# Performance work log

Measured on AMD Instinct MI355X. Metric: run time of the kernel, lower is better.

The kernel has to match this reference:

```python
import jax, jax.numpy as jnp
import numpy as np

BN_EPS = 1e-5
SQ_EPS = 1e-12


def _mlp(x, Wa, ba, g, b, Wb, bb):
    # Linear -> BatchNorm1d (eval mode, running mean=0 var=1) -> ReLU -> Linear
    h = x @ Wa + ba
    h = h * (g / jnp.sqrt(1.0 + BN_EPS)) + b
    h = jax.nn.relu(h)
    return h @ Wb + bb


def _signed_sqrt(x):
    # sqrt(relu(x)) - sqrt(relu(-x)); tiny eps keeps grads finite at exact zeros
    return jnp.sqrt(jax.nn.relu(x) + SQ_EPS) - jnp.sqrt(jax.nn.relu(-x) + SQ_EPS)


def setup_inputs() -> dict:
    G, NPG, H, POLY, L, T, TASKS, DEG = 1024, 16, 128, 16, 3, 1048576, 1, 8
    N = G * NPG
    P = G * NPG * NPG
    E = N * DEG
    key = jax.random.key(0)
    ks = iter(jax.random.split(key, 64))

    def nrm(shape, s):
        return jax.random.normal(next(ks), shape, jnp.float32) * s

    w = 0.06  # ~xavier scale for 128-dim layers
    inp = {
        'pair_x': nrm((P, POLY), 1.0),
        'diag_x': nrm((N, POLY), 1.0),
        'node_h': nrm((N, H), 1.0),
        'edge_h': nrm((E, H), 1.0),
        'W_pair': nrm((POLY, H), 0.12),
        'W_diag': nrm((POLY, H), 0.12),
        'Wd': nrm((2 * H, TASKS), w),
        'bd': jnp.zeros((TASKS,), jnp.float32),
    }
    for p, ind in (('m1', H), ('m2', H), ('up', 2 * H)):
        inp[p + '_Wa'] = nrm((L, ind, H), w)
        inp[p + '_ba'] = jnp.zeros((L, H), jnp.float32)
        inp[p + '_g'] = jnp.ones((L, H), jnp.float32)
        inp[p + '_b'] = jnp.zeros((L, H), jnp.float32)
        inp[p + '_Wb'] = nrm((L, H, H), w)
        inp[p + '_bb'] = jnp.zeros((L, H), jnp.float32)
    inp['edge_pos'] = jax.random.randint(next(ks), (E,), 0, P)
    n = jnp.arange(N)
    inp['diag_pos'] = (n // NPG) * NPG * NPG + (n % NPG) * NPG + (n % NPG)
    # graph-local triples: base pair block of the graph + random local pair ids
    tg = jax.random.randint(next(ks), (T,), 0, G) * (NPG * NPG)
    loc = jax.random.randint(next(ks), (3, T), 0, NPG * NPG)
    inp['triple_index'] = tg[None, :] + loc
    inp['batch'] = jnp.repeat(jnp.arange(G), NPG)
    inp['pair_x_batch'] = jnp.repeat(jnp.arange(G), NPG * NPG)
    inp['ptr'] = jnp.arange(G + 1) * NPG
    inp['pair_x_ptr'] = jnp.arange(G + 1) * (NPG * NPG)
    return inp


def reference(pair_x, diag_x, node_h, edge_h, W_pair, W_diag,
              m1_Wa, m1_ba, m1_g, m1_b, m1_Wb, m1_bb,
              m2_Wa, m2_ba, m2_g, m2_b, m2_Wb, m2_bb,
              up_Wa, up_ba, up_g, up_b, up_Wb, up_bb,
              Wd, bd,
              edge_pos, diag_pos, triple_index, batch, pair_x_batch, ptr, pair_x_ptr):
    P = pair_x.shape[0]
    # InitLayer: coalesce-add of pair, edge and diagonal (node) contributions
    pair_h = pair_x @ W_pair                             # [P, H]
    pair_h = pair_h.at[edge_pos].add(edge_h)
    pair_h = pair_h.at[diag_pos].add(node_h + diag_x @ W_diag)
    idx0, idx1, idx2 = triple_index[0], triple_index[1], triple_index[2]
    L = m1_Wa.shape[0]
    for l in range(L):  # fixed small layer count
        h1 = _mlp(pair_h, m1_Wa[l], m1_ba[l], m1_g[l], m1_b[l], m1_Wb[l], m1_bb[l])
        h2 = _mlp(pair_h, m2_Wa[l], m2_ba[l], m2_g[l], m2_b[l], m2_Wb[l], m2_bb[l])
        x3 = h1[idx1] * h2[idx2]                         # [T, H] gather-multiply
        agg = jax.ops.segment_sum(x3, idx0, num_segments=P)  # scatter_add
        agg = _signed_sqrt(agg)                          # use_sqrt=True
        h = jnp.concatenate([pair_h, agg], axis=-1)      # [P, 2H]
        pair_h = _mlp(h, up_Wa[l], up_ba[l], up_g[l], up_b[l], up_Wb[l], up_bb[l]) + pair_h
    G = ptr.shape[0] - 1
    agg_all = jax.ops.segment_sum(pair_h, pair_x_batch, num_segments=G)
    agg_diag = jax.ops.segment_sum(pair_h[diag_pos], batch, num_segments=G)
    agg_off = agg_all - agg_diag
    node_sz = jnp.diff(ptr)[:, None].astype(pair_h.dtype)
    pair_sz = jnp.diff(pair_x_ptr)[:, None].astype(pair_h.dtype)
    agg_off = agg_off / jnp.maximum(pair_sz - node_sz, 1.0)  # 'mean' pooling
    agg_diag = agg_diag / node_sz
    graph_h = jnp.concatenate([agg_diag, agg_off], axis=-1)  # [G, 2H]
    return graph_h @ Wd + bd                             # output decoder
```

## Files before the change

kernel.cpp:

```cpp
#include <hip/hip_runtime.h>
#include <hip/hip_bf16.h>

#define H 128
#define POLY 16
#define PPG 256
#define GNUM 1024
#define PTOT 262144
#define NTOT 16384
#define ETOT 131072
#define TTOT 1048576

#define NCHUNK 4
#define GPC (GNUM / NCHUNK)
#define ROWS (PTOT / NCHUNK)

#define NB PTOT

#define XS 136

typedef __attribute__((ext_vector_type(8))) _Float16       f16x8;
typedef __attribute__((ext_vector_type(8))) unsigned short ushort8;
typedef __attribute__((ext_vector_type(4))) float          f32x4;

__device__ __forceinline__ unsigned short f2h(float f) {
    _Float16 h = (_Float16)f;
    return __builtin_bit_cast(unsigned short, h);
}
__device__ __forceinline__ float h2f(unsigned short u) {
    _Float16 h = __builtin_bit_cast(_Float16, u);
    return (float)h;
}
__device__ __forceinline__ void split2(float x, unsigned short& h, unsigned short& l)
{
    h = f2h(x);
    l = f2h(x - h2f(h));
}
__device__ __forceinline__ f16x8 ldf16(const unsigned short* p)
{
    return __builtin_bit_cast(f16x8, *(const ushort8*)p);
}

__global__ __launch_bounds__(256)
void k_init_pair(const float* __restrict__ px, const float* __restrict__ Wp,
                 float* __restrict__ ph)
{
    const int tid = threadIdx.x;
    const int c4 = (tid & 31) * 4;
    float4 w[POLY];
#pragma unroll
    for (int k = 0; k < POLY; ++k) w[k] = *(const float4*)(Wp + k * H + c4);
    const size_t r0 = (size_t)blockIdx.x * 64 + (tid >> 5) * 8;
#pragma unroll
    for (int rr = 0; rr < 8; ++rr) {
        const size_t p = r0 + rr;
        const float4* xp = (const float4*)(px + p * POLY);
        const float4 v0 = xp[0], v1 = xp[1], v2 = xp[2], v3 = xp[3];
        const float x[POLY] = {v0.x, v0.y, v0.z, v0.w, v1.x, v1.y, v1.z, v1.w,
                               v2.x, v2.y, v2.z, v2.w, v3.x, v3.y, v3.z, v3.w};
        float4 a = make_float4(0.f, 0.f, 0.f, 0.f);
#pragma unroll
        for (int k = 0; k < POLY; ++k) {
            a.x = fmaf(x[k], w[k].x, a.x);
            a.y = fmaf(x[k], w[k].y, a.y);
            a.z = fmaf(x[k], w[k].z, a.z);
            a.w = fmaf(x[k], w[k].w, a.w);
        }
        *(float4*)(ph + p * H + c4) = a;
    }
}

__global__ __launch_bounds__(256)
void k_edge(const float* __restrict__ eh, const int* __restrict__ epos, float* ph)
{
    const int tid = threadIdx.x;
    const size_t e = (size_t)blockIdx.x * 2 + (tid >> 7);
    const int c = tid & 127;
    atomicAdd(&ph[(size_t)epos[e] * H + c], eh[e * H + c]);
}

__global__ __launch_bounds__(256)
void k_diag(const float* __restrict__ nh, const float* __restrict__ dx,
            const float* __restrict__ Wdg, const int* __restrict__ dpos, float* ph)
{
    const int tid = threadIdx.x;
    const int c4 = (tid & 31) * 4;
    float4 w[POLY];
#pragma unroll
    for (int k = 0; k < POLY; ++k) w[k] = *(const float4*)(Wdg + k * H + c4);
    const size_t n0 = (size_t)blockIdx.x * 64 + (tid >> 5) * 8;
#pragma unroll
    for (int rr = 0; rr < 8; ++rr) {
        const size_t n = n0 + rr;
        const float4* xp = (const float4*)(dx + n * POLY);
        const float4 v0 = xp[0], v1 = xp[1], v2 = xp[2], v3 = xp[3];
        const float x[POLY] = {v0.x, v0.y, v0.z, v0.w, v1.x, v1.y, v1.z, v1.w,
                               v2.x, v2.y, v2.z, v2.w, v3.x, v3.y, v3.z, v3.w};
        const float4 nv = *(const float4*)(nh + n * H + c4);
        float4 a = nv;
#pragma unroll
        for (int k = 0; k < POLY; ++k) {
            a.x = fmaf(x[k], w[k].x, a.x);
            a.y = fmaf(x[k], w[k].y, a.y);
            a.z = fmaf(x[k], w[k].z, a.z);
            a.w = fmaf(x[k], w[k].w, a.w);
        }
        float* dst = ph + (size_t)dpos[n] * H + c4;
        const float4 old = *(const float4*)dst;
        a.x += old.x; a.y += old.y; a.z += old.z; a.w += old.w;
        *(float4*)dst = a;
    }
}

__global__ __launch_bounds__(1024)
void k_zero(int* counts) { counts[blockIdx.x * 1024 + threadIdx.x] = 0; }

__global__ __launch_bounds__(256)
void k_count(const int* __restrict__ i0, int* counts)
{
    const int t = blockIdx.x * 256 + threadIdx.x;
    atomicAdd(&counts[i0[t]], 1);
}

__global__ __launch_bounds__(1024)
void k_scan1(const int* __restrict__ counts, int* __restrict__ offs, int* __restrict__ bsum)
{
    __shared__ int s[1024];
    const int t = threadIdx.x;
    const int i = blockIdx.x * 1024 + t;
    const int v = counts[i];
    s[t] = v;
    __syncthreads();
    for (int d = 1; d < 1024; d <<= 1) {
        int add = (t >= d) ? s[t - d] : 0;
        __syncthreads();
        s[t] += add;
        __syncthreads();
    }
    offs[i] = s[t] - v;
    if (t == 1023) bsum[blockIdx.x] = s[1023];
}

__global__ __launch_bounds__(256)
void k_scan2(const int* __restrict__ bsum, int* __restrict__ bbase)
{
    __shared__ int s[256];
    const int t = threadIdx.x;
    const int v = bsum[t];
    s[t] = v;
    __syncthreads();
    for (int d = 1; d < 256; d <<= 1) {
        int add = (t >= d) ? s[t - d] : 0;
        __syncthreads();
        s[t] += add;
        __syncthreads();
    }
    bbase[t] = s[t] - v;
}

__global__ __launch_bounds__(1024)
void k_scan3(int* __restrict__ offs, const int* __restrict__ bbase, int* __restrict__ cursor)
{
    const int i = blockIdx.x * 1024 + threadIdx.x;
    const int o = offs[i] + bbase[blockIdx.x];
    offs[i] = o;
    cursor[i] = o;
    if (i == 0) offs[NB] = TTOT;
}

__global__ __launch_bounds__(256)
void k_fill(const int* __restrict__ i0, const int* __restrict__ i1,
            const int* __restrict__ i2, int* cursor, unsigned short* __restrict__ tri16)
{
    const int t = blockIdx.x * 256 + threadIdx.x;
    const int a0 = i0[t];
    const int pos = atomicAdd(&cursor[a0], 1);
    tri16[pos] = (unsigned short)((i1[t] & 255) | ((i2[t] & 255) << 8));
}

__device__ __forceinline__ void stage2(const float* __restrict__ src,
                                       unsigned short* Xh, unsigned short* Xl, int tid)
{
#pragma unroll
    for (int it = 0; it < 4; ++it) {
        const int r = (tid >> 4) + it * 16;
        const int c = (tid & 15) * 8;
        const float4 v0 = *(const float4*)(src + (size_t)r * H + c);
        const float4 v1 = *(const float4*)(src + (size_t)r * H + c + 4);
        const float x[8] = {v0.x, v0.y, v0.z, v0.w, v1.x, v1.y, v1.z, v1.w};
        ushort8 vh, vl;
#pragma unroll
        for (int j = 0; j < 8; ++j) {
            unsigned short hh, ll;
            split2(x[j], hh, ll);
            vh[j] = hh; vl[j] = ll;
        }
        *(ushort8*)(Xh + r * XS + c) = vh;
        *(ushort8*)(Xl + r * XS + c) = vl;
    }
}

#define MFMA16F(A, B, C) __builtin_amdgcn_mfma_f32_16x16x32_f16(A, B, C, 0, 0, 0)

__device__ __forceinline__ void gemm2(const unsigned short* Xh, const unsigned short* Xl,
                                      const unsigned short* __restrict__ wp,
                                      const int rt, const int cb, const int lane,
                                      f32x4 (&acc)[2][4])
{
    const int arow = lane & 15, akb = (lane >> 4) * 8;
#pragma unroll
    for (int kc = 0; kc < 4; ++kc) {
        const int kin = kc * 32 + akb;
        f16x8 ah[2], al[2];
#pragma unroll
        for (int s = 0; s < 2; ++s) {
            const int ro = (rt + s * 16 + arow) * XS + kin;
            ah[s] = ldf16(Xh + ro);
            al[s] = ldf16(Xl + ro);
        }
#pragma unroll
        for (int j = 0; j < 4; ++j) {
            const unsigned short* bp = wp + (size_t)(kc * 8 + cb + j) * 1024 + lane * 8;
            const f16x8 bh = ldf16(bp);
            const f16x8 bl = ldf16(bp + 512);
#pragma unroll
            for (int s = 0; s < 2; ++s) {
                acc[s][j] = MFMA16F(ah[s], bh, acc[s][j]);
                acc[s][j] = MFMA16F(al[s], bh, acc[s][j]);
                acc[s][j] = MFMA16F(ah[s], bl, acc[s][j]);
                acc[s][j] = MFMA16F(al[s], bl, acc[s][j]);
            }
        }
    }
}

__global__ __launch_bounds__(256)
void k_mlp_m12(const float* __restrict__ x1,
               const unsigned short* __restrict__ wa1, const float* __restrict__ ba1,
               const float* __restrict__ gg1, const float* __restrict__ bsh1,
               const unsigned short* __restrict__ wb1, const float* __restrict__ bb1,
               float* __restrict__ out1,
               const unsigned short* __restrict__ wa2, const float* __restrict__ ba2,
               const float* __restrict__ gg2, const float* __restrict__ bsh2,
               const unsigned short* __restrict__ wb2, const float* __restrict__ bb2,
               float* __restrict__ out2)
{
    __shared__ unsigned short Xh[64 * XS], Xl[64 * XS];

    const int tid = threadIdx.x, lane = tid & 63, wid = tid >> 6;
    const int sel = blockIdx.x & 1;
    const size_t row0 = (size_t)(blockIdx.x >> 1) * 64;

    const unsigned short* wa = sel ? wa2 : wa1;
    const unsigned short* wb = sel ? wb2 : wb1;
    const float* ba  = sel ? ba2  : ba1;
    const float* gg  = sel ? gg2  : gg1;
    const float* bsh = sel ? bsh2 : bsh1;
    const float* bb  = sel ? bb2  : bb1;
    float* out = sel ? out2 : out1;

    const int rt = (wid >> 1) * 32;
    const int cb = (wid & 1) * 4;

    f32x4 acc[2][4];
#pragma unroll
    for (int s = 0; s < 2; ++s)
#pragma unroll
        for (int j = 0; j < 4; ++j)
#pragma unroll
            for (int q = 0; q < 4; ++q) acc[s][j][q] = 0.f;

    stage2(x1 + row0 * H, Xh, Xl, tid);
    __syncthreads();
    gemm2(Xh, Xl, wa, rt, cb, lane, acc);
    __syncthreads();

    const float inv_s = rsqrtf(1.0f + 1e-5f);
    const int crow = (lane >> 4) * 4, ccol = lane & 15;
#pragma unroll
    for (int j = 0; j < 4; ++j) {
        const int col = (cb + j) * 16 + ccol;
        const float g  = gg[col] * inv_s;
        const float a_ = ba[col];
        const float b_ = bsh[col];
#pragma unroll
        for (int s = 0; s < 2; ++s)
#pragma unroll
            for (int q = 0; q < 4; ++q) {
                float t = fmaf(acc[s][j][q] + a_, g, b_);
                t = fmaxf(t, 0.f);
                unsigned short hh, ll;
                split2(t, hh, ll);
                const int ro = (rt + s * 16 + crow + q) * XS + col;
                Xh[ro] = hh; Xl[ro] = ll;
                acc[s][j][q] = 0.f;
            }
    }
    __syncthreads();

    gemm2(Xh, Xl, wb, rt, cb, lane, acc);

#pragma unroll
    for (int j = 0; j < 4; ++j) {
        const int col = (cb + j) * 16 + ccol;
        const float bbv = bb[col];
#pragma unroll
        for (int s = 0; s < 2; ++s)
#pragma unroll
            for (int q = 0; q < 4; ++q) {
                const int row = rt + s * 16 + crow + q;
                out[(row0 + row) * H + col] = acc[s][j][q] + bbv;
            }
    }
}

__global__ __launch_bounds__(256)
void k_mlp_up(const float* __restrict__ x1, const float* __restrict__ x2,
              const unsigned short* __restrict__ wpa,
              const float* __restrict__ ba, const float* __restrict__ gg,
              const float* __restrict__ bsh,
              const unsigned short* __restrict__ wpb, const float* __restrict__ bb,
              float* __restrict__ out)
{
    __shared__ unsigned short Xh[64 * XS], Xl[64 * XS];

    const int tid = threadIdx.x, lane = tid & 63, wid = tid >> 6;
    const size_t row0 = (size_t)blockIdx.x * 64;
    const int rt = (wid >> 1) * 32;
    const int cb = (wid & 1) * 4;

    f32x4 acc[2][4];
#pragma unroll
    for (int s = 0; s < 2; ++s)
#pragma unroll
        for (int j = 0; j < 4; ++j)
#pragma unroll
            for (int q = 0; q < 4; ++q) acc[s][j][q] = 0.f;

    stage2(x1 + row0 * H, Xh, Xl, tid);
    __syncthreads();
    gemm2(Xh, Xl, wpa, rt, cb, lane, acc);
    __syncthreads();
    stage2(x2 + row0 * H, Xh, Xl, tid);
    __syncthreads();
    gemm2(Xh, Xl, wpa + 32 * 1024, rt, cb, lane, acc);
    __syncthreads();

    const float inv_s = rsqrtf(1.0f + 1e-5f);
    const int crow = (lane >> 4) * 4, ccol = lane & 15;
#pragma unroll
    for (int j = 0; j < 4; ++j) {
        const int col = (cb + j) * 16 + ccol;
        const float g  = gg[col] * inv_s;
        const float a_ = ba[col];
        const float b_ = bsh[col];
#pragma unroll
        for (int s = 0; s < 2; ++s)
#pragma unroll
            for (int q = 0; q < 4; ++q) {
                float t = fmaf(acc[s][j][q] + a_, g, b_);
                t = fmaxf(t, 0.f);
                unsigned short hh, ll;
                split2(t, hh, ll);
                const int ro = (rt + s * 16 + crow + q) * XS + col;
                Xh[ro] = hh; Xl[ro] = ll;
                acc[s][j][q] = 0.f;
            }
    }
    __syncthreads();

    gemm2(Xh, Xl, wpb, rt, cb, lane, acc);

#pragma unroll
    for (int j = 0; j < 4; ++j) {
        const int col = (cb + j) * 16 + ccol;
        const float bbv = bb[col];
#pragma unroll
        for (int s = 0; s < 2; ++s)
#pragma unroll
            for (int q = 0; q < 4; ++q) {
                const int row = rt + s * 16 + crow + q;
                float o = acc[s][j][q] + bbv + x1[(row0 + row) * H + col];
                out[(row0 + row) * H + col] = o;
            }
    }
}

__global__ __launch_bounds__(64)
void k_prepack2(const float* __restrict__ W, int lstride,
                unsigned short* __restrict__ outp, int ostride)
{
    const int l = blockIdx.y;
    const float* w = W + (size_t)l * lstride;
    unsigned short* o = outp + (size_t)l * ostride + (size_t)blockIdx.x * 1024;
    const int lane = threadIdx.x;
    const int kbase = (blockIdx.x >> 3) * 32 + (lane >> 4) * 8;
    const int col   = (blockIdx.x & 7) * 16 + (lane & 15);
    ushort8 vh, vl;
#pragma unroll
    for (int j = 0; j < 8; ++j) {
        unsigned short hh, ll;
        split2(w[(size_t)(kbase + j) * H + col], hh, ll);
        vh[j] = hh; vl[j] = ll;
    }
    *(ushort8*)(o + lane * 8)       = vh;
    *(ushort8*)(o + 512 + lane * 8) = vl;
}

__global__ __launch_bounds__(256)
void k_triple_s(const float* __restrict__ h1, const float* __restrict__ h2,
                const unsigned short* __restrict__ tri16,
                const int* __restrict__ offs,
                float* __restrict__ aggout)
{
    const int lane = threadIdx.x & 63;
    const int lp   = blockIdx.x * 4 + (threadIdx.x >> 6);
    const int start = offs[lp], end = offs[lp + 1];
    const size_t base = (size_t)(lp >> 8) * PPG * H + lane * 2;
    float ax = 0.f, ay = 0.f;
    unsigned us = (start < end) ? tri16[start] : 0u;
    for (int t = start; t < end; ++t) {
        const unsigned usn = (t + 1 < end) ? tri16[t + 1] : 0u;
        const float2 a = *(const float2*)&h1[base + (size_t)(us & 255u) * H];
        const float2 b = *(const float2*)&h2[base + (size_t)(us >> 8) * H];
        ax = fmaf(a.x, b.x, ax);
        ay = fmaf(a.y, b.y, ay);
        us = usn;
    }
    float2 r;
    r.x = sqrtf(fmaxf(ax, 0.f) + 1e-12f) - sqrtf(fmaxf(-ax, 0.f) + 1e-12f);
    r.y = sqrtf(fmaxf(ay, 0.f) + 1e-12f) - sqrtf(fmaxf(-ay, 0.f) + 1e-12f);
    *(float2*)&aggout[(size_t)lp * H + lane * 2] = r;
}

__global__ __launch_bounds__(256)
void k_pool(const float* __restrict__ ph, const float* __restrict__ Wd,
            const float* __restrict__ bd, float* __restrict__ out)
{
    const int g = blockIdx.x;
    const int tid = threadIdx.x;
    const int c = tid & 127, half = tid >> 7;
    const size_t base = (size_t)g * PPG * H;
    float s = 0.f;
    for (int r = half * 128; r < half * 128 + 128; ++r)
        s += ph[base + (size_t)r * H + c];
    __shared__ float sother[128];
    __shared__ float red[128];
    if (half) sother[c] = s;
    __syncthreads();
    if (!half) {
        const float tot = s + sother[c];
        float d = 0.f;
#pragma unroll
        for (int i = 0; i < 16; ++i)
            d += ph[base + (size_t)(i * 17) * H + c];
        const float diag = d * (1.f / 16.f);
        const float offv = (tot - d) * (1.f / 240.f);
        red[c] = fmaf(diag, Wd[c], offv * Wd[128 + c]);
    }
    __syncthreads();
    if (tid < 64) {
        float r = red[tid] + red[tid + 64];
#pragma unroll
        for (int off = 32; off; off >>= 1) r += __shfl_down(r, off);
        if (tid == 0) out[g] = r + bd[0];
    }
}

extern "C" void kernel_launch(void* const* d_in, const int* in_sizes, int n_in,
                              void* d_out, int out_size, void* d_ws, size_t ws_size,
                              hipStream_t stream)
{
    (void)in_sizes; (void)n_in; (void)out_size;
    const size_t OFF_PH  = 0;
    const size_t OFF_HA  = 134217728;
    const size_t OFF_HB  = 167772160;
    const size_t OFF_AGG = 201326592;
    const size_t OFF_TRI = 234881024;
    const size_t OFF_INT = 236978176;
    const size_t OFF_WP  = 240128000;
    const size_t NEED    = OFF_WP + 1376256;
    if (ws_size < NEED) return;

    const float* pair_x = (const float*)d_in[0];
    const float* diag_x = (const float*)d_in[1];
    const float* node_h = (const float*)d_in[2];
    const float* edge_h = (const float*)d_in[3];
    const float* W_pair = (const float*)d_in[4];
    const float* W_diag = (const float*)d_in[5];
    const float* Wd     = (const float*)d_in[6];
    const float* bd     = (const float*)d_in[7];
    const float* mW[3][6];
    for (int p = 0; p < 3; ++p)
        for (int q = 0; q < 6; ++q)
            mW[p][q] = (const float*)d_in[8 + p * 6 + q];
    const int* edge_pos = (const int*)d_in[26];
    const int* diag_pos = (const int*)d_in[27];
    const int* tri_idx  = (const int*)d_in[28];

    char* w = (char*)d_ws;
    float*          ph   = (float*)(w + OFF_PH);
    float*          hA   = (float*)(w + OFF_HA);
    float*          hB   = (float*)(w + OFF_HB);
    float*          aggC = (float*)(w + OFF_AGG);
    unsigned short* tri16 = (unsigned short*)(w + OFF_TRI);
    int*            counts = (int*)(w + OFF_INT);
    int*            offs   = counts + NB;
    int*            cursor = offs + NB + 8;
    int*            bsum   = cursor + NB;
    int*            bbase  = bsum + 256;
    unsigned short* wp   = (unsigned short*)(w + OFF_WP);

    const int WPL = 229376;

    k_init_pair<<<PTOT / 64, 256, 0, stream>>>(pair_x, W_pair, ph);
    k_edge<<<ETOT / 2, 256, 0, stream>>>(edge_h, edge_pos, ph);
    k_diag<<<NTOT / 64, 256, 0, stream>>>(node_h, diag_x, W_diag, diag_pos, ph);

    k_prepack2<<<dim3(32, 3), 64, 0, stream>>>(mW[0][0], 16384, wp + 0,      WPL);
    k_prepack2<<<dim3(32, 3), 64, 0, stream>>>(mW[0][4], 16384, wp + 32768,  WPL);
    k_prepack2<<<dim3(32, 3), 64, 0, stream>>>(mW[1][0], 16384, wp + 65536,  WPL);
    k_prepack2<<<dim3(32, 3), 64, 0, stream>>>(mW[1][4], 16384, wp + 98304,  WPL);
    k_prepack2<<<dim3(64, 3), 64, 0, stream>>>(mW[2][0], 32768, wp + 131072, WPL);
    k_prepack2<<<dim3(32, 3), 64, 0, stream>>>(mW[2][4], 16384, wp + 196608, WPL);

    k_zero<<<NB / 1024, 1024, 0, stream>>>(counts);
    k_count<<<TTOT / 256, 256, 0, stream>>>(tri_idx, counts);
    k_scan1<<<NB / 1024, 1024, 0, stream>>>(counts, offs, bsum);
    k_scan2<<<1, 256, 0, stream>>>(bsum, bbase);
    k_scan3<<<NB / 1024, 1024, 0, stream>>>(offs, bbase, cursor);
    k_fill<<<TTOT / 256, 256, 0, stream>>>(tri_idx, tri_idx + TTOT, tri_idx + 2 * TTOT,
                                           cursor, tri16);

    for (int l = 0; l < 3; ++l) {
        const unsigned short* wl = wp + (size_t)l * WPL;
        for (int c = 0; c < NCHUNK; ++c) {
            const float* phc = ph + (size_t)c * ROWS * H;
            k_mlp_m12<<<ROWS / 64 * 2, 256, 0, stream>>>(phc,
                wl + 0,      mW[0][1] + l * 128, mW[0][2] + l * 128, mW[0][3] + l * 128,
                wl + 32768,  mW[0][5] + l * 128, hA,
                wl + 65536,  mW[1][1] + l * 128, mW[1][2] + l * 128, mW[1][3] + l * 128,
                wl + 98304,  mW[1][5] + l * 128, hB);
            k_triple_s<<<ROWS / 4, 256, 0, stream>>>(hA, hB, tri16,
                                                     offs + (size_t)c * ROWS, aggC);
            k_mlp_up<<<ROWS / 64, 256, 0, stream>>>(phc, aggC,
                wl + 131072, mW[2][1] + l * 128, mW[2][2] + l * 128, mW[2][3] + l * 128,
                wl + 196608, mW[2][5] + l * 128, (float*)phc);
        }
    }
    k_pool<<<GNUM, 256, 0, stream>>>(ph, Wd, bd, (float*)d_out);
}
```

Measured before the change: 1.757 ms.

## Fuse next chunk's m1/m2 MLP with current chunk's update MLP launch

The two MLP kernels become device helper functions, and a new combined kernel is added. Its first third of blocks runs the update MLP for the current chunk and the remaining blocks run the m1/m2 MLPs for the next chunk, or for chunk 0 of the next layer. The first m1/m2 call is moved before the loop. This is meant to cut launch gaps and give the GPU more independent blocks per launch, so the update-MLP tail overlaps with the next chunk's work. The cost is more register and scheduling pressure in one larger kernel, plus more complex chunk and layer index bookkeeping.

New measurement: 1.695 ms. 3.6% less time.

```diff
diff --git a/kernel.cpp b/kernel.cpp
--- a/kernel.cpp
+++ b/kernel.cpp
@@ -233,22 +233,20 @@
     }
 }
 
-__global__ __launch_bounds__(256)
-void k_mlp_m12(const float* __restrict__ x1,
-               const unsigned short* __restrict__ wa1, const float* __restrict__ ba1,
-               const float* __restrict__ gg1, const float* __restrict__ bsh1,
-               const unsigned short* __restrict__ wb1, const float* __restrict__ bb1,
-               float* __restrict__ out1,
-               const unsigned short* __restrict__ wa2, const float* __restrict__ ba2,
-               const float* __restrict__ gg2, const float* __restrict__ bsh2,
-               const unsigned short* __restrict__ wb2, const float* __restrict__ bb2,
-               float* __restrict__ out2)
-{
-    __shared__ unsigned short Xh[64 * XS], Xl[64 * XS];
-
-    const int tid = threadIdx.x, lane = tid & 63, wid = tid >> 6;
-    const int sel = blockIdx.x & 1;
-    const size_t row0 = (size_t)(blockIdx.x >> 1) * 64;
+__device__ __forceinline__ void mlp_m12_body(int bid, const float* __restrict__ x1,
+    const unsigned short* __restrict__ wa1, const float* __restrict__ ba1,
+    const float* __restrict__ gg1, const float* __restrict__ bsh1,
+    const unsigned short* __restrict__ wb1, const float* __restrict__ bb1,
+    float* __restrict__ out1,
+    const unsigned short* __restrict__ wa2, const float* __restrict__ ba2,
+    const float* __restrict__ gg2, const float* __restrict__ bsh2,
+    const unsigned short* __restrict__ wb2, const float* __restrict__ bb2,
+    float* __restrict__ out2,
+    unsigned short* Xh, unsigned short* Xl, int tid)
+{
+    const int lane = tid & 63, wid = tid >> 6;
+    const int sel = bid & 1;
+    const size_t row0 = (size_t)(bid >> 1) * 64;
 
     const unsigned short* wa = sel ? wa2 : wa1;
     const unsigned short* wb = sel ? wb2 : wb1;
@@ -313,18 +311,16 @@
     }
 }
 
-__global__ __launch_bounds__(256)
-void k_mlp_up(const float* __restrict__ x1, const float* __restrict__ x2,
-              const unsigned short* __restrict__ wpa,
-              const float* __restrict__ ba, const float* __restrict__ gg,
-              const float* __restrict__ bsh,
-              const unsigned short* __restrict__ wpb, const float* __restrict__ bb,
-              float* __restrict__ out)
-{
-    __shared__ unsigned short Xh[64 * XS], Xl[64 * XS];
-
-    const int tid = threadIdx.x, lane = tid & 63, wid = tid >> 6;
-    const size_t row0 = (size_t)blockIdx.x * 64;
+__device__ __forceinline__ void mlp_up_body(int bid, const float* __restrict__ x1,
+    const float* __restrict__ x2,
+    const unsigned short* __restrict__ wpa, const float* __restrict__ ba,
+    const float* __restrict__ gg, const float* __restrict__ bsh,
+    const unsigned short* __restrict__ wpb, const float* __restrict__ bb,
+    float* __restrict__ out,
+    unsigned short* Xh, unsigned short* Xl, int tid)
+{
+    const int lane = tid & 63, wid = tid >> 6;
+    const size_t row0 = (size_t)bid * 64;
     const int rt = (wid >> 1) * 32;
     const int cb = (wid & 1) * 4;
 
@@ -382,6 +378,49 @@
                 float o = acc[s][j][q] + bbv + x1[(row0 + row) * H + col];
                 out[(row0 + row) * H + col] = o;
             }
+    }
+}
+
+__global__ __launch_bounds__(256)
+void k_mlp_m12(const float* x1,
+               const unsigned short* wa1, const float* ba1, const float* gg1,
+               const float* bsh1, const unsigned short* wb1, const float* bb1, float* out1,
+               const unsigned short* wa2, const float* ba2, const float* gg2,
+               const float* bsh2, const unsigned short* wb2, const float* bb2, float* out2)
+{
+    __shared__ unsigned short Xh[64 * XS], Xl[64 * XS];
+    mlp_m12_body(blockIdx.x, x1, wa1, ba1, gg1, bsh1, wb1, bb1, out1,
+                 wa2, ba2, gg2, bsh2, wb2, bb2, out2, Xh, Xl, threadIdx.x);
+}
+
+__global__ __launch_bounds__(256)
+void k_mlp_up(const float* x1, const float* x2,
+              const unsigned short* wpa, const float* ba, const float* gg,
+              const float* bsh, const unsigned short* wpb, const float* bb, float* out)
+{
+    __shared__ unsigned short Xh[64 * XS], Xl[64 * XS];
+    mlp_up_body(blockIdx.x, x1, x2, wpa, ba, gg, bsh, wpb, bb, out,
+                Xh, Xl, threadIdx.x);
+}
+
+__global__ __launch_bounds__(256)
+void k_fused(const float* ux1, const float* ux2,
+             const unsigned short* uwpa, const float* uba, const float* ugg,
+             const float* ubsh, const unsigned short* uwpb, const float* ubb, float* uout,
+             const float* mx1,
+             const unsigned short* mwa1, const float* mba1, const float* mgg1,
+             const float* mbsh1, const unsigned short* mwb1, const float* mbb1, float* mout1,
+             const unsigned short* mwa2, const float* mba2, const float* mgg2,
+             const float* mbsh2, const unsigned short* mwb2, const float* mbb2, float* mout2)
+{
+    __shared__ unsigned short Xh[64 * XS], Xl[64 * XS];
+    const int bid = blockIdx.x;
+    if (bid < ROWS / 64) {
+        mlp_up_body(bid, ux1, ux2, uwpa, uba, ugg, ubsh, uwpb, ubb, uout,
+                    Xh, Xl, threadIdx.x);
+    } else {
+        mlp_m12_body(bid - ROWS / 64, mx1, mwa1, mba1, mgg1, mbsh1, mwb1, mbb1, mout1,
+                     mwa2, mba2, mgg2, mbsh2, mwb2, mbb2, mout2, Xh, Xl, threadIdx.x);
     }
 }
 
@@ -531,20 +570,38 @@
     k_fill<<<TTOT / 256, 256, 0, stream>>>(tri_idx, tri_idx + TTOT, tri_idx + 2 * TTOT,
                                            cursor, tri16);
 
+    {
+        const unsigned short* wl = wp;
+        k_mlp_m12<<<ROWS / 64 * 2, 256, 0, stream>>>(ph,
+            wl + 0,      mW[0][1], mW[0][2], mW[0][3], wl + 32768,  mW[0][5], hA,
+            wl + 65536,  mW[1][1], mW[1][2], mW[1][3], wl + 98304,  mW[1][5], hB);
+    }
     for (int l = 0; l < 3; ++l) {
         const unsigned short* wl = wp + (size_t)l * WPL;
         for (int c = 0; c < NCHUNK; ++c) {
-            const float* phc = ph + (size_t)c * ROWS * H;
-            k_mlp_m12<<<ROWS / 64 * 2, 256, 0, stream>>>(phc,
-                wl + 0,      mW[0][1] + l * 128, mW[0][2] + l * 128, mW[0][3] + l * 128,
-                wl + 32768,  mW[0][5] + l * 128, hA,
-                wl + 65536,  mW[1][1] + l * 128, mW[1][2] + l * 128, mW[1][3] + l * 128,
-                wl + 98304,  mW[1][5] + l * 128, hB);
+            float* phc = ph + (size_t)c * ROWS * H;
             k_triple_s<<<ROWS / 4, 256, 0, stream>>>(hA, hB, tri16,
                                                      offs + (size_t)c * ROWS, aggC);
-            k_mlp_up<<<ROWS / 64, 256, 0, stream>>>(phc, aggC,
-                wl + 131072, mW[2][1] + l * 128, mW[2][2] + l * 128, mW[2][3] + l * 128,
-                wl + 196608, mW[2][5] + l * 128, (float*)phc);
+            const bool has_next = (c < NCHUNK - 1) || (l < 2);
+            if (has_next) {
+                const int nl = (c < NCHUNK - 1) ? l : l + 1;
+                const int nc = (c < NCHUNK - 1) ? c + 1 : 0;
+                const unsigned short* wn = wp + (size_t)nl * WPL;
+                float* phn = ph + (size_t)nc * ROWS * H;
+                k_fused<<<ROWS / 64 * 3, 256, 0, stream>>>(
+                    phc, aggC,
+                    wl + 131072, mW[2][1] + l * 128, mW[2][2] + l * 128,
+                    mW[2][3] + l * 128, wl + 196608, mW[2][5] + l * 128, phc,
+                    phn,
+                    wn + 0,      mW[0][1] + nl * 128, mW[0][2] + nl * 128,
+                    mW[0][3] + nl * 128, wn + 32768,  mW[0][5] + nl * 128, hA,
+                    wn + 65536,  mW[1][1] + nl * 128, mW[1][2] + nl * 128,
+                    mW[1][3] + nl * 128, wn + 98304,  mW[1][5] + nl * 128, hB);
+            } else {
+                k_mlp_up<<<ROWS / 64, 256, 0, stream>>>(phc, aggC,
+                    wl + 131072, mW[2][1] + l * 128, mW[2][2] + l * 128,
+                    mW[2][3] + l * 128, wl + 196608, mW[2][5] + l * 128, phc);
+            }
         }
     }
     k_pool<<<GNUM, 256, 0, stream>>>(ph, Wd, bd, (float*)d_out);
```
